# Kernel tuning notes

Hardware: AMD Instinct MI355X
Metric: run time of the kernel (lower is better)

Reference implementation:

```python
import jax, jax.numpy as jnp
import numpy as np

B, S, D = 512, 500, 128
NQ, NC, NQD, NCD = 10000, 500, 100, 100

def _glorot(key, shape):
    fan_in, fan_out = shape[0], shape[1]
    lim = np.sqrt(6.0 / (fan_in + fan_out))
    return jax.random.uniform(key, shape, jnp.float32, -lim, lim)

def setup_inputs() -> dict:
    key = jax.random.key(0)
    ks = jax.random.split(key, 24)
    inp = {
        'question_seq': jax.random.randint(ks[0], (B, S), 0, NQ),
        'concept_seq': jax.random.randint(ks[1], (B, S), 0, NC),
        'question_diff_seq': jax.random.randint(ks[2], (B, S), 0, NQD),
        'concept_diff_seq': jax.random.randint(ks[3], (B, S), 0, NCD),
        'correct_seq': jax.random.randint(ks[4], (B, S), 0, 2),
        # embedding tables
        'Eq': jax.random.normal(ks[5], (NQ, D), jnp.float32),
        'Ec': jax.random.normal(ks[6], (NC, D), jnp.float32),
        'Eqd': jax.random.normal(ks[7], (NQD, D), jnp.float32),
        'Ecd': jax.random.normal(ks[8], (NCD, D), jnp.float32),
        'Ecorr': jax.random.normal(ks[9], (2, D), jnp.float32),
        # linear layers (stored as [in, out], y = x @ W + b)
        'Wx': _glorot(ks[10], (4 * D, D)), 'bx': jnp.zeros((D,), jnp.float32),
        'Wsdf1': _glorot(ks[11], (D, D)), 'bsdf1': jnp.zeros((D,), jnp.float32),
        'Wsdf2': _glorot(ks[12], (D, D)), 'bsdf2': jnp.zeros((D,), jnp.float32),
        'Wpka1': _glorot(ks[13], (2 * D, D)), 'bpka1': jnp.zeros((D,), jnp.float32),
        'Wpka2': _glorot(ks[14], (2 * D, D)), 'bpka2': jnp.zeros((D,), jnp.float32),
        'Wki': _glorot(ks[15], (4 * D, D)), 'bki': jnp.zeros((D,), jnp.float32),
        # xavier_uniform init of h_pre (torch nn.init.xavier_uniform_ on zeros(B, D))
        'h0': _glorot(ks[16], (B, D)),
    }
    return inp

def reference(question_seq, concept_seq, question_diff_seq, concept_diff_seq,
              correct_seq, Eq, Ec, Eqd, Ecd, Ecorr, Wx, bx,
              Wsdf1, bsdf1, Wsdf2, bsdf2, Wpka1, bpka1, Wpka2, bpka2,
              Wki, bki, h0):
    # embed all sequences: [B, S, D]
    qe = Eq[question_seq]
    ce = Ec[concept_seq]
    qde = Eqd[question_diff_seq]
    cde = Ecd[concept_diff_seq]
    co = Ecorr[correct_seq]
    # x_t = generate_x_MLP(concat(...)) precomputed for all timesteps
    x_all = jnp.concatenate([qe, ce, qde, cde], axis=-1) @ Wx + bx  # [B, S, D]

    # time-major slices for scan over t = 0 .. S-2
    tm = lambda a: jnp.swapaxes(a, 0, 1)  # [S, B, D]
    xs = (tm(x_all)[:-1], tm(x_all)[1:], tm(co)[:-1], tm(qde)[:-1], tm(cde)[:-1])

    def step(h_pre, inputs):
        x_t, x_next, co_t, qd_t, cd_t = inputs
        input_sdf = x_t - h_pre
        sdf = jax.nn.sigmoid(input_sdf @ Wsdf1 + bsdf1) * jnp.tanh(input_sdf @ Wsdf2 + bsdf2)
        input_pka = jnp.concatenate([sdf, co_t], axis=-1)
        pka = jax.nn.sigmoid(input_pka @ Wpka1 + bpka1) * jnp.tanh(input_pka @ Wpka2 + bpka2)
        input_ki = jnp.concatenate([h_pre, co_t, qd_t, cd_t], axis=-1)
        gamma = jax.nn.sigmoid(input_ki @ Wki + bki)
        h = gamma * h_pre + (1.0 - gamma) * pka
        y_t = jax.nn.sigmoid(jnp.sum(x_next * h, axis=-1))  # [B]
        return h, y_t

    _, ys = jax.lax.scan(step, h0, xs)  # ys: [S-1, B]
    # y[:, S-1] is never written in the original (stays 0)
    y = jnp.concatenate([ys.T, jnp.zeros((question_seq.shape[0], 1), jnp.float32)], axis=1)
    return y
```

## Files before the change

kernel.cpp:

```cpp
#include <hip/hip_runtime.h>
#include <hip/hip_bf16.h>
#include <cstdint>
#include <cstddef>

#define BB 512
#define SS 500
#define TT 499
#define NRB 256
#define L2E 1.4426950408889634f

typedef float  f32x4  __attribute__((ext_vector_type(4)));
typedef short  bf16x8 __attribute__((ext_vector_type(8)));

#define MFMA16(A, B, C) __builtin_amdgcn_mfma_f32_16x16x32_bf16((A), (B), (C), 0, 0, 0)

static constexpr size_t OFF_TQ    = 0;
static constexpr size_t OFF_TC    = 10240000;
static constexpr size_t OFF_TQD   = 10752000;
static constexpr size_t OFF_TCD   = 10854400;
static constexpr size_t OFF_TCOK  = 10956800;
static constexpr size_t OFF_TP1   = 10957824;
static constexpr size_t OFF_TP2   = 10958848;
static constexpr size_t OFF_TMPA  = 10959872;
static constexpr size_t OFF_TMPB  = 11011072;
static constexpr size_t OFF_WFRAG = 11062272;
static constexpr size_t OFF_YPART = 11226112;
static constexpr size_t TOTAL_WS  = 19401728;

__device__ unsigned char g_fb[TOTAL_WS];

__device__ __forceinline__ unsigned short f2bf(float f) {
    union { float f; uint32_t u; } v; v.f = f;
    uint32_t u = v.u;
    uint32_t r = u + 0x7FFFu + ((u >> 16) & 1u);
    return (unsigned short)(r >> 16);
}
__device__ __forceinline__ float fsig(float z) {
    return __builtin_amdgcn_rcpf(1.0f + __expf(-z));
}
__device__ __forceinline__ uint32_t cvtpk(float lo, float hi) {
    uint32_t r;
    asm("v_cvt_pk_bf16_f32 %0, %1, %2" : "=v"(r) : "v"(lo), "v"(hi));
    return r;
}
__device__ __forceinline__ void bar_lgkm() {
    asm volatile("s_waitcnt lgkmcnt(0)" ::: "memory");
    __builtin_amdgcn_s_barrier();
}
__device__ __forceinline__ float sum16(float x) {
    int a = __float_as_int(x);
    int b = __builtin_amdgcn_update_dpp(a, a, 0xB1, 0xF, 0xF, false);
    float s = x + __int_as_float(b);
    int c = __float_as_int(s);
    int d = __builtin_amdgcn_update_dpp(c, c, 0x4E, 0xF, 0xF, false);
    s += __int_as_float(d);
    int e = __float_as_int(s);
    int f = __builtin_amdgcn_update_dpp(e, e, 0x141, 0xF, 0xF, false);
    s += __int_as_float(f);
    int gg = __float_as_int(s);
    int hh = __builtin_amdgcn_update_dpp(gg, gg, 0x140, 0xF, 0xF, false);
    return s + __int_as_float(hh);
}

__global__ __launch_bounds__(128) void k_tables(
    const float* __restrict__ Eq, const float* __restrict__ Ec,
    const float* __restrict__ Eqd, const float* __restrict__ Ecd,
    const float* __restrict__ Ecorr,
    const float* __restrict__ Wx,  const float* __restrict__ bx,
    const float* __restrict__ Wpka1, const float* __restrict__ bpka1,
    const float* __restrict__ Wpka2, const float* __restrict__ bpka2,
    const float* __restrict__ Wki, const float* __restrict__ bki,
    float* __restrict__ TQ, float* __restrict__ TC,
    float* __restrict__ TQD, float* __restrict__ TCD,
    float* __restrict__ TCOk, float* __restrict__ Tp1, float* __restrict__ Tp2,
    float* __restrict__ tmpA, float* __restrict__ tmpB)
{
    int blk = blockIdx.x;
    const float* A; const float* W; const float* bias = nullptr; float* out; int row;
    int ostride = 1;
    float oscale = 1.0f;
    if      (blk < 10000) { A = Eq;    row = blk;          W = Wx;              bias = bx;    out = TQ;   ostride = 2; }
    else if (blk < 10500) { A = Ec;    row = blk - 10000;  W = Wx  + 128*128;                 out = TC;   ostride = 2; }
    else if (blk < 10600) { A = Eqd;   row = blk - 10500;  W = Wx  + 256*128;                 out = TQD;  ostride = 2; }
    else if (blk < 10700) { A = Ecd;   row = blk - 10600;  W = Wx  + 384*128;                 out = TCD;  ostride = 2; }
    else if (blk < 10800) { A = Eqd;   row = blk - 10700;  W = Wki + 256*128;                 out = tmpA; }
    else if (blk < 10900) { A = Ecd;   row = blk - 10800;  W = Wki + 384*128;                 out = tmpB; }
    else if (blk < 10902) { A = Ecorr; row = blk - 10900;  W = Wki + 128*128;   bias = bki;   out = TCOk; oscale = -L2E; }
    else if (blk < 10904) { A = Ecorr; row = blk - 10902;  W = Wpka1 + 128*128; bias = bpka1; out = Tp1;  oscale = -L2E; }
    else                  { A = Ecorr; row = blk - 10904;  W = Wpka2 + 128*128; bias = bpka2; out = Tp2;  oscale = -2.0f*L2E; }

    __shared__ float a[128];
    int c = threadIdx.x;
    a[c] = A[row * 128 + c];
    __syncthreads();
    float acc = bias ? bias[c] : 0.0f;
    #pragma unroll 8
    for (int k = 0; k < 128; ++k) acc += a[k] * W[k * 128 + c];
    out[(size_t)(row * 128 + c) * ostride] = acc * oscale;
}

__global__ __launch_bounds__(128) void k_tables2(
    const float* __restrict__ Wki,
    float* __restrict__ TQ, float* __restrict__ TC,
    float* __restrict__ TQD, float* __restrict__ TCD,
    const float* __restrict__ tmpA, const float* __restrict__ tmpB)
{
    int blk = blockIdx.x;
    float* base2; const float* tmp = nullptr; int row;
    if      (blk < 10000) { row = blk;          base2 = TQ  + (size_t)row * 256; }
    else if (blk < 10500) { row = blk - 10000;  base2 = TC  + (size_t)row * 256; }
    else if (blk < 10600) { row = blk - 10500;  base2 = TQD + (size_t)row * 256; tmp = tmpA + (size_t)row * 128; }
    else                  { row = blk - 10600;  base2 = TCD + (size_t)row * 256; tmp = tmpB + (size_t)row * 128; }
    __shared__ float a[128];
    int c = threadIdx.x;
    a[c] = base2[c * 2];
    __syncthreads();
    float acc = tmp ? tmp[c] : 0.0f;
    #pragma unroll 8
    for (int k = 0; k < 128; ++k) acc += a[k] * Wki[k * 128 + c];
    base2[c * 2 + 1] = acc * (-L2E);
}

__global__ __launch_bounds__(64) void k_wfrag(
    const float* __restrict__ Wsdf1, const float* __restrict__ Wsdf2,
    const float* __restrict__ Wpka1, const float* __restrict__ Wpka2,
    const float* __restrict__ Wki, unsigned short* __restrict__ wfrag)
{
    int bid = blockIdx.x;
    int m = bid >> 5, w = (bid >> 2) & 7, kt = bid & 3;
    const float* W = (m == 0) ? Wsdf1 : (m == 1) ? Wsdf2 : (m == 2) ? Wpka1 : (m == 3) ? Wpka2 : Wki;
    float sgn = (m == 0) ? -L2E : (m == 1) ? -2.0f*L2E : (m == 2) ? -L2E : (m == 3) ? -2.0f*L2E : L2E;
    int l = threadIdx.x;
    int cc = w * 16 + (l & 15);
    int k0 = kt * 32 + ((l >> 4) << 3);
    unsigned short v[8];
    #pragma unroll
    for (int j = 0; j < 8; ++j) v[j] = f2bf(sgn * W[(size_t)(k0 + j) * 128 + cc]);
    unsigned short* dst = wfrag + ((( (size_t)m * 8 + w) * 4 + kt) * 64 + l) * 8;
    #pragma unroll
    for (int j = 0; j < 8; ++j) dst[j] = v[j];
}

__global__ __launch_bounds__(512, 2) void k_rec(
    const int* __restrict__ qs, const int* __restrict__ cs,
    const int* __restrict__ qds, const int* __restrict__ cds, const int* __restrict__ corr,
    const float2* __restrict__ TQ, const float2* __restrict__ TC,
    const float2* __restrict__ TQD, const float2* __restrict__ TCD,
    const float* __restrict__ TCOk,
    const unsigned short* __restrict__ wfrag,
    const float* __restrict__ Tp1, const float* __restrict__ Tp2,
    const float* __restrict__ bsdf1, const float* __restrict__ bsdf2,
    const float* __restrict__ h0, float* __restrict__ ypart)
{
    int rb = blockIdx.x;
    int tid = threadIdx.x;
    int w = tid >> 6, l = tid & 63;
    int g = l >> 4, cl = l & 15;
    int col = w * 16 + cl;
    int row = g & 1;
    bool owner = (g < 2);

    __shared__ __align__(16) unsigned short dbuf[256];
    __shared__ __align__(16) unsigned short sbuf[256];

    bf16x8 wf[5][4];
    #pragma unroll
    for (int m = 0; m < 5; ++m)
        #pragma unroll
        for (int kt = 0; kt < 4; ++kt)
            wf[m][kt] = *(const bf16x8*)(wfrag + ((((size_t)m * 8 + w) * 4 + kt) * 64 + l) * 8);

    float bs1 = bsdf1[col] * (-L2E);
    float bs2 = bsdf2[col] * (-2.0f * L2E);
    float tp1a = Tp1[col], tp1b = Tp1[128 + col];
    float tp2a = Tp2[col], tp2b = Tp2[128 + col];

    float h = h0[(size_t)(rb * 2 + row) * 128 + col];

    char* pdw = (char*)dbuf + row * 256 + ((col * 2) ^ (row << 6));
    char* psw = (char*)sbuf + row * 256 + ((col * 2) ^ (row << 6));
    const bf16x8* prd[4]; const bf16x8* prs[4];
    int rrow = cl & 1;
    #pragma unroll
    for (int kt = 0; kt < 4; ++kt) {
        int off = rrow * 256 + ((kt * 64 + g * 16) ^ (rrow << 6));
        prd[kt] = (const bf16x8*)((char*)dbuf + off);
        prs[kt] = (const bf16x8*)((char*)sbuf + off);
    }

    int boff = (rb * 2 + row) * SS;

    float* ypt = ypart + (size_t)rb * 16 + w * 2 + row;
    const size_t YSTR = (size_t)NRB * 16;
    bool ystore = (owner && cl == 0);

    float x1, kip0, kip1; unsigned int c0, c1;
    {
        int o0 = boff;
        int iq = qs[o0], ic = cs[o0], iqd = qds[o0], icd = cds[o0], ico = corr[o0];
        float2 q = TQ[(size_t)iq * 128 + col], c_ = TC[(size_t)ic * 128 + col];
        float2 qd = TQD[(size_t)iqd * 128 + col], cd = TCD[(size_t)icd * 128 + col];
        float co = TCOk[(size_t)ico * 128 + col];
        float x0 = q.x + c_.x + qd.x + cd.x;
        kip0 = q.y + c_.y + qd.y + cd.y + co;
        c0 = (unsigned int)ico & 1u;
        uint32_t pk = cvtpk(x0 - h, x0 - h);
        if (owner) *(unsigned short*)pdw = (unsigned short)pk;
    }
    {
        int o1 = boff + 1;
        int iq = qs[o1], ic = cs[o1], iqd = qds[o1], icd = cds[o1], ico = corr[o1];
        float2 q = TQ[(size_t)iq * 128 + col], c_ = TC[(size_t)ic * 128 + col];
        float2 qd = TQD[(size_t)iqd * 128 + col], cd = TCD[(size_t)icd * 128 + col];
        float co = TCOk[(size_t)ico * 128 + col];
        x1 = q.x + c_.x + qd.x + cd.x;
        kip1 = q.y + c_.y + qd.y + cd.y + co;
        c1 = (unsigned int)ico & 1u;
    }
    bar_lgkm();

    #pragma unroll 2
    for (int t = 0; t < TT; ++t) {
        int tp = t + 2; tp = (tp > 499) ? 499 : tp;
        int op = boff + tp;
        int iq = qs[op], ic = cs[op], iqd = qds[op], icd = cds[op], ico = corr[op];
        float2 gq = TQ[(size_t)iq * 128 + col], gc = TC[(size_t)ic * 128 + col];
        float2 gqd = TQD[(size_t)iqd * 128 + col], gcd = TCD[(size_t)icd * 128 + col];
        float gco = TCOk[(size_t)ico * 128 + col];

        f32x4 s1a = {bs1, bs1, bs1, bs1}, s1b = {0.f, 0.f, 0.f, 0.f};
        f32x4 s2a = {bs2, bs2, bs2, bs2}, s2b = {0.f, 0.f, 0.f, 0.f};
        f32x4 gda = {0.f, 0.f, 0.f, 0.f}, gdb = {0.f, 0.f, 0.f, 0.f};
        {
            bf16x8 d0 = *prd[0], d1 = *prd[1], d2 = *prd[2], d3 = *prd[3];
            s1a = MFMA16(d0, wf[0][0], s1a); s2a = MFMA16(d0, wf[1][0], s2a); gda = MFMA16(d0, wf[4][0], gda);
            s1b = MFMA16(d2, wf[0][2], s1b); s2b = MFMA16(d2, wf[1][2], s2b); gdb = MFMA16(d2, wf[4][2], gdb);
            s1a = MFMA16(d1, wf[0][1], s1a); s2a = MFMA16(d1, wf[1][1], s2a); gda = MFMA16(d1, wf[4][1], gda);
            s1b = MFMA16(d3, wf[0][3], s1b); s2b = MFMA16(d3, wf[1][3], s2b); gdb = MFMA16(d3, wf[4][3], gdb);
        }
        float s1v = (row ? s1a[1] : s1a[0]) + (row ? s1b[1] : s1b[0]);
        float s2v = (row ? s2a[1] : s2a[0]) + (row ? s2b[1] : s2b[0]);
        float gdv = (row ? gda[1] : gda[0]) + (row ? gdb[1] : gdb[0]);
        float gv = __builtin_amdgcn_rcpf(1.0f + __builtin_amdgcn_exp2f(gdv + kip0));
        float e1 = __builtin_amdgcn_exp2f(s1v), e2 = __builtin_amdgcn_exp2f(s2v);
        float sdf = (1.0f - e2) * __builtin_amdgcn_rcpf((1.0f + e1) * (1.0f + e2));
        {
            uint32_t pk = cvtpk(sdf, sdf);
            if (owner) *(unsigned short*)psw = (unsigned short)pk;
        }
        bar_lgkm();

        f32x4 p1a = {0.f, 0.f, 0.f, 0.f}, p1b = {0.f, 0.f, 0.f, 0.f};
        f32x4 p2a = {0.f, 0.f, 0.f, 0.f}, p2b = {0.f, 0.f, 0.f, 0.f};
        {
            bf16x8 f0 = *prs[0], f1 = *prs[1], f2 = *prs[2], f3 = *prs[3];
            p1a = MFMA16(f0, wf[2][0], p1a); p2a = MFMA16(f0, wf[3][0], p2a);
            p1b = MFMA16(f2, wf[2][2], p1b); p2b = MFMA16(f2, wf[3][2], p2b);
            p1a = MFMA16(f1, wf[2][1], p1a); p2a = MFMA16(f1, wf[3][1], p2a);
            p1b = MFMA16(f3, wf[2][3], p1b); p2b = MFMA16(f3, wf[3][3], p2b);
        }
        float p1v = (row ? p1a[1] : p1a[0]) + (row ? p1b[1] : p1b[0]);
        float p2v = (row ? p2a[1] : p2a[0]) + (row ? p2b[1] : p2b[0]);
        float t1 = c0 ? tp1b : tp1a;
        float t2 = c0 ? tp2b : tp2a;
        float e1p = __builtin_amdgcn_exp2f(p1v + t1), e2p = __builtin_amdgcn_exp2f(p2v + t2);
        float pka = (1.0f - e2p) * __builtin_amdgcn_rcpf((1.0f + e1p) * (1.0f + e2p));
        h = gv * (h - pka) + pka;

        {
            uint32_t pk = cvtpk(x1 - h, x1 - h);
            if (owner) *(unsigned short*)pdw = (unsigned short)pk;
        }
        float yv = sum16(x1 * h);
        if (ystore) ypt[0] = yv;
        ypt += YSTR;
        bar_lgkm();

        x1 = gq.x + gc.x + gqd.x + gcd.x;
        kip0 = kip1;
        kip1 = gq.y + gc.y + gqd.y + gcd.y + gco;
        c0 = c1;
        c1 = (unsigned int)ico & 1u;
    }
}

__global__ __launch_bounds__(256) void k_yfinal(const float* __restrict__ ypart, float* __restrict__ y)
{
    int id = blockIdx.x * 256 + threadIdx.x;
    if (id >= BB * SS) return;
    int b = id / SS, t = id - b * SS;
    if (t == TT) { y[id] = 0.0f; return; }
    int rb = b >> 1, pair = b & 1;
    const float* base = ypart + (size_t)t * NRB * 16 + (size_t)rb * 16 + pair;
    float s = 0.0f;
    #pragma unroll
    for (int w = 0; w < 8; ++w) s += base[w * 2];
    y[id] = fsig(s);
}

extern "C" void kernel_launch(void* const* d_in, const int* in_sizes, int n_in,
                              void* d_out, int out_size, void* d_ws, size_t ws_size,
                              hipStream_t stream) {
    const int* qs    = (const int*)d_in[0];
    const int* cs    = (const int*)d_in[1];
    const int* qds   = (const int*)d_in[2];
    const int* cds   = (const int*)d_in[3];
    const int* corr  = (const int*)d_in[4];
    const float* Eq    = (const float*)d_in[5];
    const float* Ec    = (const float*)d_in[6];
    const float* Eqd   = (const float*)d_in[7];
    const float* Ecd   = (const float*)d_in[8];
    const float* Ecorr = (const float*)d_in[9];
    const float* Wx    = (const float*)d_in[10];
    const float* bx    = (const float*)d_in[11];
    const float* Wsdf1 = (const float*)d_in[12];
    const float* bsdf1 = (const float*)d_in[13];
    const float* Wsdf2 = (const float*)d_in[14];
    const float* bsdf2 = (const float*)d_in[15];
    const float* Wpka1 = (const float*)d_in[16];
    const float* bpka1 = (const float*)d_in[17];
    const float* Wpka2 = (const float*)d_in[18];
    const float* bpka2 = (const float*)d_in[19];
    const float* Wki   = (const float*)d_in[20];
    const float* bki   = (const float*)d_in[21];
    const float* h0    = (const float*)d_in[22];

    char* base;
    if (ws_size >= TOTAL_WS) {
        base = (char*)d_ws;
    } else {
        void* p = nullptr;
        hipGetSymbolAddress(&p, HIP_SYMBOL(g_fb));
        base = (char*)p;
    }

    float* TQ    = (float*)(base + OFF_TQ);
    float* TC    = (float*)(base + OFF_TC);
    float* TQD   = (float*)(base + OFF_TQD);
    float* TCD   = (float*)(base + OFF_TCD);
    float* TCOk  = (float*)(base + OFF_TCOK);
    float* Tp1   = (float*)(base + OFF_TP1);
    float* Tp2   = (float*)(base + OFF_TP2);
    float* tmpA  = (float*)(base + OFF_TMPA);
    float* tmpB  = (float*)(base + OFF_TMPB);
    unsigned short* wfrag = (unsigned short*)(base + OFF_WFRAG);
    float* ypart = (float*)(base + OFF_YPART);

    k_tables<<<10906, 128, 0, stream>>>(Eq, Ec, Eqd, Ecd, Ecorr, Wx, bx,
                                        Wpka1, bpka1, Wpka2, bpka2, Wki, bki,
                                        TQ, TC, TQD, TCD, TCOk, Tp1, Tp2, tmpA, tmpB);
    k_tables2<<<10700, 128, 0, stream>>>(Wki, TQ, TC, TQD, TCD, tmpA, tmpB);
    k_wfrag<<<160, 64, 0, stream>>>(Wsdf1, Wsdf2, Wpka1, Wpka2, Wki, wfrag);
    k_rec<<<NRB, 512, 0, stream>>>(qs, cs, qds, cds, corr,
                                   (const float2*)TQ, (const float2*)TC,
                                   (const float2*)TQD, (const float2*)TCD, TCOk,
                                   wfrag, Tp1, Tp2, bsdf1, bsdf2, h0, ypart);
    k_yfinal<<<(BB * SS + 255) / 256, 256, 0, stream>>>(ypart, (float*)d_out);
}
```

Baseline: 530.9 us.

## Pre-gather per-step inputs into a stream buffer and run one batch row per block

Adds a k_gather kernel that performs all embedding-table gathers and sums ahead of time into a time-major float2 stream (~263MB) plus a packed correctness byte array. The recurrent kernel then reads one coalesced float2 per step instead of five indices and five dependent table lookups. Each block now handles a single batch row (512 blocks, launch bounds raised to 4 waves), doubling parallelism across CUs at the cost of wasting MFMA rows. The tradeoff is a large extra write/read of streamed data through HBM and one more kernel launch.

```diff
diff --git a/kernel.cpp b/kernel.cpp
--- a/kernel.cpp
+++ b/kernel.cpp
@@ -6,7 +6,7 @@
 #define BB 512
 #define SS 500
 #define TT 499
-#define NRB 256
+#define NRB 512
 #define L2E 1.4426950408889634f
 
 typedef float  f32x4  __attribute__((ext_vector_type(4)));
@@ -24,8 +24,10 @@
 static constexpr size_t OFF_TMPA  = 10959872;
 static constexpr size_t OFF_TMPB  = 11011072;
 static constexpr size_t OFF_WFRAG = 11062272;
-static constexpr size_t OFF_YPART = 11226112;
-static constexpr size_t TOTAL_WS  = 19401728;
+static constexpr size_t OFF_CPK   = 11226112;
+static constexpr size_t OFF_STRM  = 11488256;
+static constexpr size_t OFF_YPART = 274680832;
+static constexpr size_t TOTAL_WS  = 282856448;
 
 __device__ unsigned char g_fb[TOTAL_WS];
 
@@ -141,27 +143,57 @@
     for (int j = 0; j < 8; ++j) dst[j] = v[j];
 }
 
-__global__ __launch_bounds__(512, 2) void k_rec(
+__global__ __launch_bounds__(512) void k_gather(
     const int* __restrict__ qs, const int* __restrict__ cs,
     const int* __restrict__ qds, const int* __restrict__ cds, const int* __restrict__ corr,
     const float2* __restrict__ TQ, const float2* __restrict__ TC,
     const float2* __restrict__ TQD, const float2* __restrict__ TCD,
     const float* __restrict__ TCOk,
+    float2* __restrict__ strm, unsigned char* __restrict__ cpk)
+{
+    int bid = blockIdx.x;
+    int t = bid >> 7, chunk = bid & 127;
+    int tid = threadIdx.x;
+    int b = chunk * 4 + (tid >> 7);
+    int col = tid & 127;
+
+    int iq  = qs  [(size_t)b * SS + t];
+    int ic  = cs  [(size_t)b * SS + t];
+    int iqd = qds [(size_t)b * SS + t];
+    int icd = cds [(size_t)b * SS + t];
+    int ico = corr[(size_t)b * SS + t];
+
+    float2 q  = TQ [(size_t)iq  * 128 + col];
+    float2 c_ = TC [(size_t)ic  * 128 + col];
+    float2 qd = TQD[(size_t)iqd * 128 + col];
+    float2 cd = TCD[(size_t)icd * 128 + col];
+    float  co = TCOk[(size_t)ico * 128 + col];
+
+    float2 o;
+    o.x = q.x + c_.x + qd.x + cd.x;
+    o.y = q.y + c_.y + qd.y + cd.y + co;
+    strm[((size_t)t * BB + b) * 128 + col] = o;
+
+    if (col == 0) cpk[(size_t)b * 512 + t] = (unsigned char)(ico & 1);
+}
+
+__global__ __launch_bounds__(512, 4) void k_rec(
+    const float2* __restrict__ strm, const unsigned char* __restrict__ cpkg,
     const unsigned short* __restrict__ wfrag,
     const float* __restrict__ Tp1, const float* __restrict__ Tp2,
     const float* __restrict__ bsdf1, const float* __restrict__ bsdf2,
     const float* __restrict__ h0, float* __restrict__ ypart)
 {
-    int rb = blockIdx.x;
+    int b = blockIdx.x;
     int tid = threadIdx.x;
     int w = tid >> 6, l = tid & 63;
     int g = l >> 4, cl = l & 15;
     int col = w * 16 + cl;
-    int row = g & 1;
-    bool owner = (g < 2);
-
-    __shared__ __align__(16) unsigned short dbuf[256];
-    __shared__ __align__(16) unsigned short sbuf[256];
+    bool owner = (g == 0);
+    bool ystore = (l == 0);
+
+    __shared__ __align__(16) unsigned short dbuf[128];
+    __shared__ __align__(16) unsigned short sbuf[128];
 
     bf16x8 wf[5][4];
     #pragma unroll
@@ -175,72 +207,52 @@
     float tp1a = Tp1[col], tp1b = Tp1[128 + col];
     float tp2a = Tp2[col], tp2b = Tp2[128 + col];
 
-    float h = h0[(size_t)(rb * 2 + row) * 128 + col];
-
-    char* pdw = (char*)dbuf + row * 256 + ((col * 2) ^ (row << 6));
-    char* psw = (char*)sbuf + row * 256 + ((col * 2) ^ (row << 6));
-    const bf16x8* prd[4]; const bf16x8* prs[4];
-    int rrow = cl & 1;
-    #pragma unroll
-    for (int kt = 0; kt < 4; ++kt) {
-        int off = rrow * 256 + ((kt * 64 + g * 16) ^ (rrow << 6));
-        prd[kt] = (const bf16x8*)((char*)dbuf + off);
-        prs[kt] = (const bf16x8*)((char*)sbuf + off);
-    }
-
-    int boff = (rb * 2 + row) * SS;
-
-    float* ypt = ypart + (size_t)rb * 16 + w * 2 + row;
-    const size_t YSTR = (size_t)NRB * 16;
-    bool ystore = (owner && cl == 0);
+    float h = h0[(size_t)b * 128 + col];
+
+    char* pdw = (char*)dbuf + col * 2;
+    char* psw = (char*)sbuf + col * 2;
+    const char* rd = (const char*)dbuf + g * 16;
+    const char* rs = (const char*)sbuf + g * 16;
+
+    const size_t TSTR2 = (size_t)BB * 128;
+    const float2* sp = strm + (size_t)b * 128 + col;
+    const unsigned char* cp = cpkg + (size_t)b * 512;
 
     float x1, kip0, kip1; unsigned int c0, c1;
     {
-        int o0 = boff;
-        int iq = qs[o0], ic = cs[o0], iqd = qds[o0], icd = cds[o0], ico = corr[o0];
-        float2 q = TQ[(size_t)iq * 128 + col], c_ = TC[(size_t)ic * 128 + col];
-        float2 qd = TQD[(size_t)iqd * 128 + col], cd = TCD[(size_t)icd * 128 + col];
-        float co = TCOk[(size_t)ico * 128 + col];
-        float x0 = q.x + c_.x + qd.x + cd.x;
-        kip0 = q.y + c_.y + qd.y + cd.y + co;
-        c0 = (unsigned int)ico & 1u;
-        uint32_t pk = cvtpk(x0 - h, x0 - h);
+        float2 p0 = sp[0];
+        float2 p1 = sp[TSTR2];
+        kip0 = p0.y; x1 = p1.x; kip1 = p1.y;
+        c0 = cp[0] & 1u; c1 = cp[1] & 1u;
+        uint32_t pk = cvtpk(p0.x - h, p0.x - h);
         if (owner) *(unsigned short*)pdw = (unsigned short)pk;
     }
-    {
-        int o1 = boff + 1;
-        int iq = qs[o1], ic = cs[o1], iqd = qds[o1], icd = cds[o1], ico = corr[o1];
-        float2 q = TQ[(size_t)iq * 128 + col], c_ = TC[(size_t)ic * 128 + col];
-        float2 qd = TQD[(size_t)iqd * 128 + col], cd = TCD[(size_t)icd * 128 + col];
-        float co = TCOk[(size_t)ico * 128 + col];
-        x1 = q.x + c_.x + qd.x + cd.x;
-        kip1 = q.y + c_.y + qd.y + cd.y + co;
-        c1 = (unsigned int)ico & 1u;
-    }
     bar_lgkm();
+
+    float* ypt = ypart + (size_t)b * 8 + w;
+    const size_t YSTR = (size_t)BB * 8;
 
     #pragma unroll 2
     for (int t = 0; t < TT; ++t) {
-        int tp = t + 2; tp = (tp > 499) ? 499 : tp;
-        int op = boff + tp;
-        int iq = qs[op], ic = cs[op], iqd = qds[op], icd = cds[op], ico = corr[op];
-        float2 gq = TQ[(size_t)iq * 128 + col], gc = TC[(size_t)ic * 128 + col];
-        float2 gqd = TQD[(size_t)iqd * 128 + col], gcd = TCD[(size_t)icd * 128 + col];
-        float gco = TCOk[(size_t)ico * 128 + col];
+        float2 p2 = sp[(size_t)(t + 2) * TSTR2];
+        unsigned int cN = cp[t + 2] & 1u;
 
         f32x4 s1a = {bs1, bs1, bs1, bs1}, s1b = {0.f, 0.f, 0.f, 0.f};
         f32x4 s2a = {bs2, bs2, bs2, bs2}, s2b = {0.f, 0.f, 0.f, 0.f};
         f32x4 gda = {0.f, 0.f, 0.f, 0.f}, gdb = {0.f, 0.f, 0.f, 0.f};
         {
-            bf16x8 d0 = *prd[0], d1 = *prd[1], d2 = *prd[2], d3 = *prd[3];
+            bf16x8 d0 = *(const bf16x8*)(rd +   0);
+            bf16x8 d1 = *(const bf16x8*)(rd +  64);
+            bf16x8 d2 = *(const bf16x8*)(rd + 128);
+            bf16x8 d3 = *(const bf16x8*)(rd + 192);
             s1a = MFMA16(d0, wf[0][0], s1a); s2a = MFMA16(d0, wf[1][0], s2a); gda = MFMA16(d0, wf[4][0], gda);
             s1b = MFMA16(d2, wf[0][2], s1b); s2b = MFMA16(d2, wf[1][2], s2b); gdb = MFMA16(d2, wf[4][2], gdb);
             s1a = MFMA16(d1, wf[0][1], s1a); s2a = MFMA16(d1, wf[1][1], s2a); gda = MFMA16(d1, wf[4][1], gda);
             s1b = MFMA16(d3, wf[0][3], s1b); s2b = MFMA16(d3, wf[1][3], s2b); gdb = MFMA16(d3, wf[4][3], gdb);
         }
-        float s1v = (row ? s1a[1] : s1a[0]) + (row ? s1b[1] : s1b[0]);
-        float s2v = (row ? s2a[1] : s2a[0]) + (row ? s2b[1] : s2b[0]);
-        float gdv = (row ? gda[1] : gda[0]) + (row ? gdb[1] : gdb[0]);
+        float s1v = s1a[0] + s1b[0];
+        float s2v = s2a[0] + s2b[0];
+        float gdv = gda[0] + gdb[0];
         float gv = __builtin_amdgcn_rcpf(1.0f + __builtin_amdgcn_exp2f(gdv + kip0));
         float e1 = __builtin_amdgcn_exp2f(s1v), e2 = __builtin_amdgcn_exp2f(s2v);
         float sdf = (1.0f - e2) * __builtin_amdgcn_rcpf((1.0f + e1) * (1.0f + e2));
@@ -253,14 +265,17 @@
         f32x4 p1a = {0.f, 0.f, 0.f, 0.f}, p1b = {0.f, 0.f, 0.f, 0.f};
         f32x4 p2a = {0.f, 0.f, 0.f, 0.f}, p2b = {0.f, 0.f, 0.f, 0.f};
         {
-            bf16x8 f0 = *prs[0], f1 = *prs[1], f2 = *prs[2], f3 = *prs[3];
+            bf16x8 f0 = *(const bf16x8*)(rs +   0);
+            bf16x8 f1 = *(const bf16x8*)(rs +  64);
+            bf16x8 f2 = *(const bf16x8*)(rs + 128);
+            bf16x8 f3 = *(const bf16x8*)(rs + 192);
             p1a = MFMA16(f0, wf[2][0], p1a); p2a = MFMA16(f0, wf[3][0], p2a);
             p1b = MFMA16(f2, wf[2][2], p1b); p2b = MFMA16(f2, wf[3][2], p2b);
             p1a = MFMA16(f1, wf[2][1], p1a); p2a = MFMA16(f1, wf[3][1], p2a);
             p1b = MFMA16(f3, wf[2][3], p1b); p2b = MFMA16(f3, wf[3][3], p2b);
         }
-        float p1v = (row ? p1a[1] : p1a[0]) + (row ? p1b[1] : p1b[0]);
-        float p2v = (row ? p2a[1] : p2a[0]) + (row ? p2b[1] : p2b[0]);
+        float p1v = p1a[0] + p1b[0];
+        float p2v = p2a[0] + p2b[0];
         float t1 = c0 ? tp1b : tp1a;
         float t2 = c0 ? tp2b : tp2a;
         float e1p = __builtin_amdgcn_exp2f(p1v + t1), e2p = __builtin_amdgcn_exp2f(p2v + t2);
@@ -276,11 +291,7 @@
         ypt += YSTR;
         bar_lgkm();
 
-        x1 = gq.x + gc.x + gqd.x + gcd.x;
-        kip0 = kip1;
-        kip1 = gq.y + gc.y + gqd.y + gcd.y + gco;
-        c0 = c1;
-        c1 = (unsigned int)ico & 1u;
+        kip0 = kip1; x1 = p2.x; kip1 = p2.y; c0 = c1; c1 = cN;
     }
 }
 
@@ -290,11 +301,10 @@
     if (id >= BB * SS) return;
     int b = id / SS, t = id - b * SS;
     if (t == TT) { y[id] = 0.0f; return; }
-    int rb = b >> 1, pair = b & 1;
-    const float* base = ypart + (size_t)t * NRB * 16 + (size_t)rb * 16 + pair;
+    const float* base = ypart + ((size_t)t * BB + b) * 8;
     float s = 0.0f;
     #pragma unroll
-    for (int w = 0; w < 8; ++w) s += base[w * 2];
+    for (int w = 0; w < 8; ++w) s += base[w];
     y[id] = fsig(s);
 }
 
@@ -344,6 +354,8 @@
     float* tmpA  = (float*)(base + OFF_TMPA);
     float* tmpB  = (float*)(base + OFF_TMPB);
     unsigned short* wfrag = (unsigned short*)(base + OFF_WFRAG);
+    unsigned char*  cpk   = (unsigned char*)(base + OFF_CPK);
+    float2* strm = (float2*)(base + OFF_STRM);
     float* ypart = (float*)(base + OFF_YPART);
 
     k_tables<<<10906, 128, 0, stream>>>(Eq, Ec, Eqd, Ecd, Ecorr, Wx, bx,
@@ -351,9 +363,11 @@
                                         TQ, TC, TQD, TCD, TCOk, Tp1, Tp2, tmpA, tmpB);
     k_tables2<<<10700, 128, 0, stream>>>(Wki, TQ, TC, TQD, TCD, tmpA, tmpB);
     k_wfrag<<<160, 64, 0, stream>>>(Wsdf1, Wsdf2, Wpka1, Wpka2, Wki, wfrag);
-    k_rec<<<NRB, 512, 0, stream>>>(qs, cs, qds, cds, corr,
-                                   (const float2*)TQ, (const float2*)TC,
-                                   (const float2*)TQD, (const float2*)TCD, TCOk,
-                                   wfrag, Tp1, Tp2, bsdf1, bsdf2, h0, ypart);
+    k_gather<<<SS * 128, 512, 0, stream>>>(qs, cs, qds, cds, corr,
+                                           (const float2*)TQ, (const float2*)TC,
+                                           (const float2*)TQD, (const float2*)TCD, TCOk,
+                                           strm, cpk);
+    k_rec<<<NRB, 512, 0, stream>>>(strm, cpk, wfrag, Tp1, Tp2,
+                                   bsdf1, bsdf2, h0, ypart);
     k_yfinal<<<(BB * SS + 255) / 256, 256, 0, stream>>>(ypart, (float*)d_out);
 }
```

Result: slower. 1.453 ms (+173.7%).

## Fuse output sigmoid reduction into recurrent kernel and drop partial-sum buffer

Applied to the files above, without the earlier changes.

The per-wave partial dot products are now reduced through a small double-buffered LDS array inside the recurrent kernel. One thread per row sums them, applies the sigmoid and writes y directly, one step late. This removes the separate finalize kernel launch and the large global partial-sum buffer with its write and read traffic. The gather prefetch distance also drops from two steps to one, which shortens the register pipeline but leaves less time to hide the embedding-gather latency within each step.

```diff
diff --git a/kernel.cpp b/kernel.cpp
--- a/kernel.cpp
+++ b/kernel.cpp
@@ -24,8 +24,7 @@
 static constexpr size_t OFF_TMPA  = 10959872;
 static constexpr size_t OFF_TMPB  = 11011072;
 static constexpr size_t OFF_WFRAG = 11062272;
-static constexpr size_t OFF_YPART = 11226112;
-static constexpr size_t TOTAL_WS  = 19401728;
+static constexpr size_t TOTAL_WS  = 11226112;
 
 __device__ unsigned char g_fb[TOTAL_WS];
 
@@ -150,7 +149,7 @@
     const unsigned short* __restrict__ wfrag,
     const float* __restrict__ Tp1, const float* __restrict__ Tp2,
     const float* __restrict__ bsdf1, const float* __restrict__ bsdf2,
-    const float* __restrict__ h0, float* __restrict__ ypart)
+    const float* __restrict__ h0, float* __restrict__ y)
 {
     int rb = blockIdx.x;
     int tid = threadIdx.x;
@@ -162,6 +161,7 @@
 
     __shared__ __align__(16) unsigned short dbuf[256];
     __shared__ __align__(16) unsigned short sbuf[256];
+    __shared__ __align__(16) float ybuf[2][2][8];
 
     bf16x8 wf[5][4];
     #pragma unroll
@@ -189,40 +189,25 @@
     }
 
     int boff = (rb * 2 + row) * SS;
-
-    float* ypt = ypart + (size_t)rb * 16 + w * 2 + row;
-    const size_t YSTR = (size_t)NRB * 16;
-    bool ystore = (owner && cl == 0);
-
-    float x1, kip0, kip1; unsigned int c0, c1;
+    float* yrow = y + (size_t)(rb * 2) * SS;
+
+    float kip_c, x_c_unused; unsigned int c_c;
     {
-        int o0 = boff;
-        int iq = qs[o0], ic = cs[o0], iqd = qds[o0], icd = cds[o0], ico = corr[o0];
+        int iq = qs[boff], ic = cs[boff], iqd = qds[boff], icd = cds[boff], ico = corr[boff];
         float2 q = TQ[(size_t)iq * 128 + col], c_ = TC[(size_t)ic * 128 + col];
         float2 qd = TQD[(size_t)iqd * 128 + col], cd = TCD[(size_t)icd * 128 + col];
         float co = TCOk[(size_t)ico * 128 + col];
         float x0 = q.x + c_.x + qd.x + cd.x;
-        kip0 = q.y + c_.y + qd.y + cd.y + co;
-        c0 = (unsigned int)ico & 1u;
+        kip_c = q.y + c_.y + qd.y + cd.y + co;
+        c_c = (unsigned int)ico & 1u;
         uint32_t pk = cvtpk(x0 - h, x0 - h);
         if (owner) *(unsigned short*)pdw = (unsigned short)pk;
     }
-    {
-        int o1 = boff + 1;
-        int iq = qs[o1], ic = cs[o1], iqd = qds[o1], icd = cds[o1], ico = corr[o1];
-        float2 q = TQ[(size_t)iq * 128 + col], c_ = TC[(size_t)ic * 128 + col];
-        float2 qd = TQD[(size_t)iqd * 128 + col], cd = TCD[(size_t)icd * 128 + col];
-        float co = TCOk[(size_t)ico * 128 + col];
-        x1 = q.x + c_.x + qd.x + cd.x;
-        kip1 = q.y + c_.y + qd.y + cd.y + co;
-        c1 = (unsigned int)ico & 1u;
-    }
     bar_lgkm();
 
     #pragma unroll 2
     for (int t = 0; t < TT; ++t) {
-        int tp = t + 2; tp = (tp > 499) ? 499 : tp;
-        int op = boff + tp;
+        int op = boff + t + 1;
         int iq = qs[op], ic = cs[op], iqd = qds[op], icd = cds[op], ico = corr[op];
         float2 gq = TQ[(size_t)iq * 128 + col], gc = TC[(size_t)ic * 128 + col];
         float2 gqd = TQD[(size_t)iqd * 128 + col], gcd = TCD[(size_t)icd * 128 + col];
@@ -241,7 +226,7 @@
         float s1v = (row ? s1a[1] : s1a[0]) + (row ? s1b[1] : s1b[0]);
         float s2v = (row ? s2a[1] : s2a[0]) + (row ? s2b[1] : s2b[0]);
         float gdv = (row ? gda[1] : gda[0]) + (row ? gdb[1] : gdb[0]);
-        float gv = __builtin_amdgcn_rcpf(1.0f + __builtin_amdgcn_exp2f(gdv + kip0));
+        float gv = __builtin_amdgcn_rcpf(1.0f + __builtin_amdgcn_exp2f(gdv + kip_c));
         float e1 = __builtin_amdgcn_exp2f(s1v), e2 = __builtin_amdgcn_exp2f(s2v);
         float sdf = (1.0f - e2) * __builtin_amdgcn_rcpf((1.0f + e1) * (1.0f + e2));
         {
@@ -249,6 +234,12 @@
             if (owner) *(unsigned short*)psw = (unsigned short)pk;
         }
         bar_lgkm();
+
+        if (t > 0 && w == 0 && l < 2) {
+            const float* yb = ybuf[(t - 1) & 1][l];
+            float s = (yb[0] + yb[1]) + (yb[2] + yb[3]) + (yb[4] + yb[5]) + (yb[6] + yb[7]);
+            yrow[(size_t)l * SS + (t - 1)] = fsig(s);
+        }
 
         f32x4 p1a = {0.f, 0.f, 0.f, 0.f}, p1b = {0.f, 0.f, 0.f, 0.f};
         f32x4 p2a = {0.f, 0.f, 0.f, 0.f}, p2b = {0.f, 0.f, 0.f, 0.f};
@@ -261,41 +252,31 @@
         }
         float p1v = (row ? p1a[1] : p1a[0]) + (row ? p1b[1] : p1b[0]);
         float p2v = (row ? p2a[1] : p2a[0]) + (row ? p2b[1] : p2b[0]);
-        float t1 = c0 ? tp1b : tp1a;
-        float t2 = c0 ? tp2b : tp2a;
+        float t1 = c_c ? tp1b : tp1a;
+        float t2 = c_c ? tp2b : tp2a;
         float e1p = __builtin_amdgcn_exp2f(p1v + t1), e2p = __builtin_amdgcn_exp2f(p2v + t2);
         float pka = (1.0f - e2p) * __builtin_amdgcn_rcpf((1.0f + e1p) * (1.0f + e2p));
         h = gv * (h - pka) + pka;
 
+        float xn = gq.x + gc.x + gqd.x + gcd.x;
         {
-            uint32_t pk = cvtpk(x1 - h, x1 - h);
+            uint32_t pk = cvtpk(xn - h, xn - h);
             if (owner) *(unsigned short*)pdw = (unsigned short)pk;
         }
-        float yv = sum16(x1 * h);
-        if (ystore) ypt[0] = yv;
-        ypt += YSTR;
+        float yv = sum16(xn * h);
+        if (owner && cl == 0) ybuf[t & 1][row][w] = yv;
         bar_lgkm();
 
-        x1 = gq.x + gc.x + gqd.x + gcd.x;
-        kip0 = kip1;
-        kip1 = gq.y + gc.y + gqd.y + gcd.y + gco;
-        c0 = c1;
-        c1 = (unsigned int)ico & 1u;
-    }
-}
-
-__global__ __launch_bounds__(256) void k_yfinal(const float* __restrict__ ypart, float* __restrict__ y)
-{
-    int id = blockIdx.x * 256 + threadIdx.x;
-    if (id >= BB * SS) return;
-    int b = id / SS, t = id - b * SS;
-    if (t == TT) { y[id] = 0.0f; return; }
-    int rb = b >> 1, pair = b & 1;
-    const float* base = ypart + (size_t)t * NRB * 16 + (size_t)rb * 16 + pair;
-    float s = 0.0f;
-    #pragma unroll
-    for (int w = 0; w < 8; ++w) s += base[w * 2];
-    y[id] = fsig(s);
+        kip_c = gq.y + gc.y + gqd.y + gcd.y + gco;
+        c_c = (unsigned int)ico & 1u;
+    }
+
+    if (w == 0 && l < 2) {
+        const float* yb = ybuf[(TT - 1) & 1][l];
+        float s = (yb[0] + yb[1]) + (yb[2] + yb[3]) + (yb[4] + yb[5]) + (yb[6] + yb[7]);
+        yrow[(size_t)l * SS + (TT - 1)] = fsig(s);
+        yrow[(size_t)l * SS + TT] = 0.0f;
+    }
 }
 
 extern "C" void kernel_launch(void* const* d_in, const int* in_sizes, int n_in,
@@ -344,7 +325,6 @@
     float* tmpA  = (float*)(base + OFF_TMPA);
     float* tmpB  = (float*)(base + OFF_TMPB);
     unsigned short* wfrag = (unsigned short*)(base + OFF_WFRAG);
-    float* ypart = (float*)(base + OFF_YPART);
 
     k_tables<<<10906, 128, 0, stream>>>(Eq, Ec, Eqd, Ecd, Ecorr, Wx, bx,
                                         Wpka1, bpka1, Wpka2, bpka2, Wki, bki,
@@ -354,6 +334,5 @@
     k_rec<<<NRB, 512, 0, stream>>>(qs, cs, qds, cds, corr,
                                    (const float2*)TQ, (const float2*)TC,
                                    (const float2*)TQD, (const float2*)TCD, TCOk,
-                                   wfrag, Tp1, Tp2, bsdf1, bsdf2, h0, ypart);
-    k_yfinal<<<(BB * SS + 255) / 256, 256, 0, stream>>>(ypart, (float*)d_out);
-}
+                                   wfrag, Tp1, Tp2, bsdf1, bsdf2, h0, (float*)d_out);
+}
```

Result: no change. 527.5 us (-0.7%).
